# Optimization experiments

Measured on AMD Instinct MI355X. Metric: run time of the kernel, lower is better.

Reference implementation:

```python
import jax, jax.numpy as jnp
import numpy as np
from jax import lax

RATIOS = (0.5, 1.0, 2.0)
SCALES = (8, 16, 32)
BASE = 16
STRIDE = 16
N_PRE = 6000
N_POST = 300      # post-NMS proposals kept
NMS_THRESH = 0.7
MIN_SIZE = 16.0


def _anchor_base():
    x = y = BASE / 2.0
    ab = np.zeros((len(RATIOS) * len(SCALES), 4), np.float32)
    for i, r in enumerate(RATIOS):
        for j, s in enumerate(SCALES):
            h = BASE * s * np.sqrt(r)
            w = BASE * s * np.sqrt(1.0 / r)
            k = i * len(SCALES) + j
            ab[k] = [y - h / 2, x - w / 2, y + h / 2, x + w / 2]
    return ab


def _anchors(h, w):
    ab = _anchor_base()
    sy = np.arange(0, h * STRIDE, STRIDE)
    sx = np.arange(0, w * STRIDE, STRIDE)
    sx, sy = np.meshgrid(sx, sy)
    shift = np.stack((sy.ravel(), sx.ravel(), sy.ravel(), sx.ravel()), axis=1)
    # [K, A, 4] -> [K*A, 4], row-major over (y, x) pixels matching NHWC flatten
    return (ab[None, :, :] + shift[:, None, :]).reshape(-1, 4).astype(np.float32)


def _conv(x, w, b, pad):
    y = lax.conv_general_dilated(x, w, (1, 1), ((pad, pad), (pad, pad)),
                                 dimension_numbers=('NCHW', 'OIHW', 'NCHW'))
    return y + b[None, :, None, None]


def _loc2bbox(anchor, loc):
    h = anchor[:, 2] - anchor[:, 0]
    w = anchor[:, 3] - anchor[:, 1]
    cy = anchor[:, 0] + 0.5 * h
    cx = anchor[:, 1] + 0.5 * w
    dy, dx, dh, dw = loc[:, 0], loc[:, 1], loc[:, 2], loc[:, 3]
    ncy = dy * h + cy
    ncx = dx * w + cx
    nh = jnp.exp(dh) * h
    nw = jnp.exp(dw) * w
    return jnp.stack([ncy - 0.5 * nh, ncx - 0.5 * nw, ncy + 0.5 * nh, ncx + 0.5 * nw], axis=1)


def _iou(b):
    tl = jnp.maximum(b[:, None, :2], b[None, :, :2])
    br = jnp.minimum(b[:, None, 2:], b[None, :, 2:])
    wh = jnp.clip(br - tl, 0.0)
    inter = wh[..., 0] * wh[..., 1]
    area = (b[:, 2] - b[:, 0]) * (b[:, 3] - b[:, 1])
    return inter / (area[:, None] + area[None, :] - inter + 1e-9)


def _nms_keep(iou):
    # greedy NMS over score-sorted boxes: suppress later boxes overlapping kept earlier ones
    n = iou.shape[0]
    idx = jnp.arange(n)
    def step(keep, i):
        sup = (iou[i] > NMS_THRESH) & (idx > i) & keep[i]
        return keep & (~sup), None
    keep, _ = lax.scan(step, jnp.ones((n,), dtype=bool), idx)
    return keep


def _proposal(loc, fg, anchor, img_h, img_w, scale=1.0):
    boxes = _loc2bbox(anchor, loc)
    boxes = jnp.stack([jnp.clip(boxes[:, 0], 0.0, img_h),
                       jnp.clip(boxes[:, 1], 0.0, img_w),
                       jnp.clip(boxes[:, 2], 0.0, img_h),
                       jnp.clip(boxes[:, 3], 0.0, img_w)], axis=1)
    hs = boxes[:, 2] - boxes[:, 0]
    ws = boxes[:, 3] - boxes[:, 1]
    ms = MIN_SIZE * scale
    score = jnp.where((hs >= ms) & (ws >= ms), fg, -jnp.inf)
    top, idx = lax.top_k(score, N_PRE)
    bk = boxes[idx]                                    # [N_PRE, 4]
    keep = _nms_keep(_iou(lax.stop_gradient(bk)))      # selection is non-differentiable
    fs = jnp.where(keep, top, -jnp.inf)
    _, o2 = lax.top_k(fs, N_POST)
    return bk[o2]                                      # [N_POST, 4]


def setup_inputs() -> dict:
    key = jax.random.key(0)
    ks = jax.random.split(key, 4)
    C, H, W = 512, 50, 76
    return {
        "feature": jax.random.normal(ks[0], (1, C, H, W), jnp.float32),
        "conv1_w": jax.random.normal(ks[1], (512, C, 3, 3), jnp.float32) * 0.01,
        "conv1_b": jnp.zeros((512,), jnp.float32),
        "score_w": jax.random.normal(ks[2], (18, 512, 1, 1), jnp.float32) * 0.01,
        "score_b": jnp.zeros((18,), jnp.float32),
        "loc_w": jax.random.normal(ks[3], (36, 512, 1, 1), jnp.float32) * 0.01,
        "loc_b": jnp.zeros((36,), jnp.float32),
        "img_h": 800,
        "img_w": 1216,
    }


def reference(feature, conv1_w, conv1_b, score_w, score_b, loc_w, loc_b, img_h, img_w):
    _, c, h, w = feature.shape
    A = 9
    anchor = jnp.asarray(_anchors(h, w))
    x = jax.nn.relu(_conv(feature, conv1_w, conv1_b, 1))
    locs = _conv(x, loc_w, loc_b, 0)
    rpn_locs = locs.transpose(0, 2, 3, 1).reshape(1, -1, 4)
    sc = _conv(x, score_w, score_b, 0).transpose(0, 2, 3, 1)   # [1, h, w, 2A]
    sm = jax.nn.softmax(sc.reshape(1, h, w, A, 2), axis=-1)
    fg = sm[..., 1].reshape(-1)
    rpn_scores = sc.reshape(1, -1, 2)
    rois = _proposal(rpn_locs[0], fg, anchor, float(img_h), float(img_w), scale=1.0)
    return rpn_locs, rpn_scores, rois, anchor
```

## Files before the change

### kernel.cpp

```cpp
#include <hip/hip_runtime.h>

#define HH 50
#define WW2 76
#define NPIX 3800
#define CIN 512
#define NANCH 34200
#define NPRE 6000
#define NPOST 300
#define WPR 94

typedef unsigned long long u64;
typedef unsigned int u32;

__device__ __forceinline__ int PADL(int i) { return i + (i >> 4); }

template <bool DOW>
__global__ __launch_bounds__(256) void rpn_wtrans(const float* __restrict__ wgt,
                                                  float* __restrict__ wt,
                                                  const float* __restrict__ sw,
                                                  const float* __restrict__ lw,
                                                  float* __restrict__ wt2,
                                                  u32* __restrict__ hist,
                                                  u32* __restrict__ info) {
    __shared__ float tile[32][33];
    const int bx = blockIdx.x;
    const int by = blockIdx.y;
    const int t  = threadIdx.x;
    const int tx = t & 31, ty = t >> 5;
    int gid = (by * 144 + bx) * 256 + t;
    if (gid < 65536) hist[gid] = 0u;
    else if (gid < 65552) info[gid - 65536] = 0u;
    if (gid < 32768) {
        int c = gid >> 6, n = gid & 63;
        float v = 0.f;
        if (n < 18) v = sw[n * 512 + c];
        else if (n < 54) v = lw[(n - 18) * 512 + c];
        wt2[((c >> 2) * 64 + n) * 4 + (c & 3)] = v;
    }
    if (!DOW) return;
#pragma unroll
    for (int r = 0; r < 32; r += 8) {
        int ko = by * 32 + ty + r;
        tile[ty + r][tx] = wgt[(size_t)ko * 4608 + bx * 32 + tx];
    }
    __syncthreads();
#pragma unroll
    for (int r = 0; r < 32; r += 8) {
        int cit = bx * 32 + ty + r;
        wt[(size_t)cit * 512 + by * 32 + tx] = tile[tx][ty + r];
    }
}

template <bool USEWT>
__global__ __launch_bounds__(256, 4) void rpn_conv1(
    const float* __restrict__ feat, const float* __restrict__ wsrc,
    float* __restrict__ Xp, int cin_blk) {
    const int yb = blockIdx.x;
    const int kg = blockIdx.y;
    const int cz = blockIdx.z;
    const int t  = threadIdx.x;
    const int kp = t & 31;
    const int ty = t >> 5;
    const int row  = ty >> 2;
    const int xseg = ty & 3;
    const int x0 = xseg * 20;
    __shared__ float in_l[2816];
    __shared__ float w_l[4608];

    const int y0 = yb * 2 - 1;
    int inSrc[11]; u32 inValid = 0, inPad = 0;
#pragma unroll
    for (int k = 0; k < 11; ++k) {
        int q = t + k * 256;
        int c = q / 336, rem = q - c * 336;
        int r = rem / 84, xx = rem - r * 84;
        int gy = y0 + r, gx = xx - 1;
        bool inb = q < 2688;
        bool ok = inb && ((unsigned)gy < 50u) && ((unsigned)gx < 76u);
        inSrc[k] = c * NPIX + gy * 76 + gx;
        if (ok) inValid |= (1u << k);
        else if (inb) inPad |= (1u << k);
    }
#pragma unroll
    for (int k = 0; k < 11; ++k)
        if ((inPad >> k) & 1) in_l[t + k * 256] = 0.f;

    const float* wb;
    int wOffA = 0;
    int wSrc[18];
    if (USEWT) {
        wb = wsrc + (size_t)(cz * cin_blk) * 9 * 512 + kg * 64;
        wOffA = 8 * t - 7 * (t & 63);
    } else {
        wb = wsrc + (size_t)(kg * 64) * 4608 + (size_t)(cz * cin_blk) * 9;
#pragma unroll
        for (int k = 0; k < 18; ++k) {
            int q = t + k * 256;
            int c = q / 576, r2 = q - c * 576;
            int tap = r2 >> 6, ko = r2 & 63;
            wSrc[k] = ko * 4608 + c * 9 + tap;
        }
    }

    const float* fb = feat + (size_t)(cz * cin_blk) * NPIX;
    float acc0[20], acc1[20];
#pragma unroll
    for (int p = 0; p < 20; ++p) { acc0[p] = 0.f; acc1[p] = 0.f; }

    const int niter = cin_blk >> 3;
#pragma unroll 1
    for (int it = 0; it < niter; ++it) {
        __syncthreads();
#pragma unroll
        for (int k = 0; k < 11; ++k)
            if ((inValid >> k) & 1) in_l[t + k * 256] = fb[inSrc[k]];
        if (USEWT) {
#pragma unroll
            for (int k = 0; k < 18; ++k)
                w_l[t + k * 256] = wb[wOffA + k * 2048];
        } else {
#pragma unroll
            for (int k = 0; k < 18; ++k)
                w_l[t + k * 256] = wb[wSrc[k]];
        }
        __syncthreads();
#pragma unroll 1
        for (int c = 0; c < 8; ++c) {
            const float* ir0 = &in_l[(c * 4 + row) * 84 + x0];
            const float* wl  = &w_l[c * 576 + 2 * kp];
#pragma unroll
            for (int r = 0; r < 3; ++r) {
                const float* ir = ir0 + r * 84;
                float win[22];
#pragma unroll
                for (int w = 0; w < 22; ++w) win[w] = ir[w];
                float w00 = wl[(r * 3 + 0) * 64],     w01 = wl[(r * 3 + 1) * 64],     w02 = wl[(r * 3 + 2) * 64];
                float w10 = wl[(r * 3 + 0) * 64 + 1], w11 = wl[(r * 3 + 1) * 64 + 1], w12 = wl[(r * 3 + 2) * 64 + 1];
#pragma unroll
                for (int p = 0; p < 20; ++p) {
                    acc0[p] = fmaf(w00, win[p],     acc0[p]);
                    acc0[p] = fmaf(w01, win[p + 1], acc0[p]);
                    acc0[p] = fmaf(w02, win[p + 2], acc0[p]);
                    acc1[p] = fmaf(w10, win[p],     acc1[p]);
                    acc1[p] = fmaf(w11, win[p + 1], acc1[p]);
                    acc1[p] = fmaf(w12, win[p + 2], acc1[p]);
                }
            }
        }
        fb += 8 * NPIX;
        wb += USEWT ? 8 * 9 * 512 : 72;
    }

    const int k0 = kg * 64 + 2 * kp;
    const int y = yb * 2 + row;
    float* d0 = Xp + ((size_t)cz * 512 + k0) * NPIX + y * 76 + x0;
#pragma unroll
    for (int p = 0; p < 20; p += 2) {
        if (x0 + p + 1 < 76) {
            *reinterpret_cast<float2*>(d0 + p)        = make_float2(acc0[p], acc0[p + 1]);
            *reinterpret_cast<float2*>(d0 + NPIX + p) = make_float2(acc1[p], acc1[p + 1]);
        }
    }
}

__global__ __launch_bounds__(256) void rpn_combine(
    const float* __restrict__ Xp, const float* __restrict__ bias,
    float* __restrict__ Xt, int nz) {
    const int p0 = blockIdx.x * 256;
    const int c0 = blockIdx.y * 16;
    const int t  = threadIdx.x;
    __shared__ float s[16][257];
    const int p = p0 + t;
#pragma unroll 4
    for (int i = 0; i < 16; ++i) {
        float v = 0.f;
        if (p < NPIX) {
            size_t base = (size_t)(c0 + i) * NPIX + p;
            float a = bias[c0 + i];
            for (int z = 0; z < nz; ++z) a += Xp[(size_t)z * 512 * NPIX + base];
            v = fmaxf(a, 0.f);
        }
        s[i][t] = v;
    }
    __syncthreads();
    const int cs = (t & 3) * 4;
    const int pr = t >> 2;
#pragma unroll
    for (int q = 0; q < 4; ++q) {
        int p2 = p0 + pr + q * 64;
        if (p2 < NPIX) {
            int pi = pr + q * 64;
            float4 v = make_float4(s[cs][pi], s[cs + 1][pi], s[cs + 2][pi], s[cs + 3][pi]);
            *reinterpret_cast<float4*>(&Xt[(size_t)p2 * 512 + c0 + cs]) = v;
        }
    }
}

__global__ __launch_bounds__(64) void rpn_head(
    const float* __restrict__ Xt, const float* __restrict__ wt2,
    const float* __restrict__ sb, const float* __restrict__ lb,
    const int* __restrict__ ihp, const int* __restrict__ iwp,
    float* __restrict__ out, float* __restrict__ boxes,
    u32* __restrict__ keys, u32* __restrict__ hist) {
    const int p0 = blockIdx.x * 8;
    const int t  = threadIdx.x;
    __shared__ __align__(16) float xs[8 * 512];
    __shared__ float ovl[8][64];
    const float4* src = reinterpret_cast<const float4*>(Xt + (size_t)p0 * 512);
    float4* dst = reinterpret_cast<float4*>(xs);
#pragma unroll
    for (int i = 0; i < 16; ++i) dst[t + i * 64] = src[t + i * 64];
    __syncthreads();
    float acc[8];
    {
        float b = (t < 18) ? sb[t] : ((t < 54) ? lb[t - 18] : 0.f);
#pragma unroll
        for (int px = 0; px < 8; ++px) acc[px] = b;
    }
    const float4* wv = reinterpret_cast<const float4*>(wt2) + t;
#pragma unroll 4
    for (int c4 = 0; c4 < 128; ++c4) {
        float4 w = wv[c4 * 64];
#pragma unroll
        for (int px = 0; px < 8; ++px) {
            float4 x = *reinterpret_cast<const float4*>(xs + px * 512 + c4 * 4);
            acc[px] = fmaf(w.x, x.x, acc[px]);
            acc[px] = fmaf(w.y, x.y, acc[px]);
            acc[px] = fmaf(w.z, x.z, acc[px]);
            acc[px] = fmaf(w.w, x.w, acc[px]);
        }
    }
#pragma unroll
    for (int px = 0; px < 8; ++px) ovl[px][t] = acc[px];
    __syncthreads();
    const float ch = (float)(*ihp), cw = (float)(*iwp);
#pragma unroll
    for (int pass = 0; pass < 2; ++pass) {
        int a, px;
        bool act;
        if (pass == 0) { act = (t < 63); px = t / 9; a = t - px * 9; }
        else           { act = (t < 9);  px = 7;     a = t; }
        if (act) {
            const int p = p0 + px;
            const float* ov = ovl[px];
            const float s0 = ov[2 * a], s1 = ov[2 * a + 1];
            const float dy = ov[18 + 4 * a], dx = ov[18 + 4 * a + 1];
            const float dh = ov[18 + 4 * a + 2], dw = ov[18 + 4 * a + 3];
            const int yy = p / WW2, xx = p % WW2;
            const int ai = p * 9 + a;
            *reinterpret_cast<float4*>(out + ai * 4) = make_float4(dy, dx, dh, dw);
            *reinterpret_cast<float2*>(out + 136800 + ai * 2) = make_float2(s0, s1);
            double r  = (a < 3) ? 0.5 : (a < 6) ? 1.0 : 2.0;
            int m3 = a % 3;
            double s2 = (m3 == 0) ? 8.0 : (m3 == 1) ? 16.0 : 32.0;
            double hd = (16.0 * s2) * sqrt(r);
            double wd = (16.0 * s2) * sqrt(1.0 / r);
            float ay1 = (float)(8.0 - hd * 0.5), ax1 = (float)(8.0 - wd * 0.5);
            float ay2 = (float)(8.0 + hd * 0.5), ax2 = (float)(8.0 + wd * 0.5);
            float fy = (float)(yy * 16), fx = (float)(xx * 16);
            float A0 = ay1 + fy, A1 = ax1 + fx, A2 = ay2 + fy, A3 = ax2 + fx;
            *reinterpret_cast<float4*>(out + 206400 + ai * 4) = make_float4(A0, A1, A2, A3);
            float ah = __fsub_rn(A2, A0), aw = __fsub_rn(A3, A1);
            float cy = __fadd_rn(A0, __fmul_rn(0.5f, ah));
            float cx = __fadd_rn(A1, __fmul_rn(0.5f, aw));
            float ncy = __fadd_rn(__fmul_rn(dy, ah), cy);
            float ncx = __fadd_rn(__fmul_rn(dx, aw), cx);
            float nh = __fmul_rn(expf(dh), ah);
            float nw = __fmul_rn(expf(dw), aw);
            float b0 = __fsub_rn(ncy, __fmul_rn(0.5f, nh));
            float b1 = __fsub_rn(ncx, __fmul_rn(0.5f, nw));
            float b2 = __fadd_rn(ncy, __fmul_rn(0.5f, nh));
            float b3 = __fadd_rn(ncx, __fmul_rn(0.5f, nw));
            b0 = fminf(fmaxf(b0, 0.f), ch); b2 = fminf(fmaxf(b2, 0.f), ch);
            b1 = fminf(fmaxf(b1, 0.f), cw); b3 = fminf(fmaxf(b3, 0.f), cw);
            float hs = __fsub_rn(b2, b0), wsz = __fsub_rn(b3, b1);
            float m = fmaxf(s0, s1);
            float e0 = expf(__fsub_rn(s0, m)), e1 = expf(__fsub_rn(s1, m));
            float fg = __fdiv_rn(e1, __fadd_rn(e0, e1));
            float score = (hs >= 16.f && wsz >= 16.f) ? fg : -__builtin_inff();
            *reinterpret_cast<float4*>(boxes + ai * 4) = make_float4(b0, b1, b2, b3);
            u32 kb = __float_as_uint(score);
            kb = (kb & 0x80000000u) ? ~kb : (kb | 0x80000000u);
            keys[ai] = kb;
            atomicAdd(&hist[kb >> 16], 1u);
        }
    }
}

__global__ __launch_bounds__(1024) void rpn_threshsel(const u32* __restrict__ hist,
                                                      u32* __restrict__ info,
                                                      const u32* __restrict__ keys,
                                                      u64* __restrict__ selk) {
    __shared__ u32 tmp[1024];
    __shared__ u32 part[256], h2[256];
    __shared__ int segs;
    __shared__ u32 Tsh;
    const int t = threadIdx.x;
    {
        u32 s = 0;
        const u32* hp = hist + t * 64;
#pragma unroll 8
        for (int b = 0; b < 64; ++b) s += hp[b];
        tmp[t] = s;
    }
    __syncthreads();
    if (t < 256) part[t] = tmp[4 * t] + tmp[4 * t + 1] + tmp[4 * t + 2] + tmp[4 * t + 3];
    __syncthreads();
    for (int off = 1; off < 256; off <<= 1) {
        u32 v = 0, add = 0;
        if (t < 256) { v = part[t]; add = (t + off < 256) ? part[t + off] : 0u; }
        __syncthreads();
        if (t < 256) part[t] = v + add;
        __syncthreads();
    }
    if (t < 256) {
        u32 suf  = part[t];
        u32 sufn = (t < 255) ? part[t + 1] : 0u;
        if (suf >= NPRE && sufn < NPRE) segs = t;
    }
    __syncthreads();
    const int seg = segs;
    const u32 above = (seg < 255) ? part[seg + 1] : 0u;
    if (t < 256) h2[t] = hist[seg * 256 + t];
    __syncthreads();
    for (int off = 1; off < 256; off <<= 1) {
        u32 v = 0, add = 0;
        if (t < 256) { v = h2[t]; add = (t + off < 256) ? h2[t + off] : 0u; }
        __syncthreads();
        if (t < 256) h2[t] = v + add;
        __syncthreads();
    }
    if (t < 256) {
        u32 tot  = above + h2[t];
        u32 totn = above + ((t < 255) ? h2[t + 1] : 0u);
        if (tot >= NPRE && totn < NPRE) Tsh = (u32)(seg * 256 + t);
    }
    __syncthreads();
    const u32 T = Tsh;
    const int lane = t & 63;
    for (int base = 0; base < NANCH; base += 1024) {
        int idx = base + t;
        u32 k = (idx < NANCH) ? keys[idx] : 0u;
        bool sel = (idx < NANCH) && ((k >> 16) >= T);
        u64 ball = __ballot(sel);
        u32 wbase = 0;
        if (lane == 0 && ball) wbase = atomicAdd(&info[2], (u32)__popcll(ball));
        wbase = __shfl(wbase, 0);
        if (sel) {
            u32 pos = wbase + (u32)__popcll(ball & ((1ull << lane) - 1ull));
            if (pos < 8192) selk[pos] = ((u64)k << 32) | (u64)(0xFFFFFFFFu - (u32)idx);
        }
    }
}

__global__ __launch_bounds__(1024) void rpn_sort_local(u64* __restrict__ selk,
                                                       const u32* __restrict__ info) {
    __shared__ u64 s[2176];
    const int t = threadIdx.x;
    const int seg = blockIdx.x;
    const int base = seg * 2048;
    int n = (int)info[2]; if (n > 8192) n = 8192;
    for (int i = t; i < 2048; i += 1024)
        s[PADL(i)] = (base + i < n) ? selk[base + i] : 0ull;
    __syncthreads();
    const bool D = ((seg & 1) == 0);
    for (int k = 2; k <= 2048; k <<= 1) {
        for (int j = k >> 1; j > 0; j >>= 1) {
            int p1 = ((t & ~(j - 1)) << 1) | (t & (j - 1));
            int p2 = p1 | j;
            bool desc = (((p1 & k) == 0) == D);
            u64 A = s[PADL(p1)], B = s[PADL(p2)];
            if (desc ? (A < B) : (A > B)) { s[PADL(p1)] = B; s[PADL(p2)] = A; }
            __syncthreads();
        }
    }
    for (int i = t; i < 2048; i += 1024) selk[base + i] = s[PADL(i)];
}

__global__ __launch_bounds__(1024) void rpn_sort_merge(const u64* __restrict__ selk,
                                                       const float* __restrict__ boxes,
                                                       float* __restrict__ bk) {
    __shared__ u64 s[8192];
    const int t = threadIdx.x;
    for (int i = t; i < 8192; i += 1024) s[i] = selk[i];
    __syncthreads();
    for (int j = 2048; j > 0; j >>= 1) {
#pragma unroll 4
        for (int z = 0; z < 4; ++z) {
            int pi = t + z * 1024;
            int p1 = ((pi & ~(j - 1)) << 1) | (pi & (j - 1));
            int p2 = p1 | j;
            bool desc = ((p1 & 4096) == 0);
            u64 A = s[p1], B = s[p2];
            if (desc ? (A < B) : (A > B)) { s[p1] = B; s[p2] = A; }
        }
        __syncthreads();
    }
    for (int j = 4096; j > 0; j >>= 1) {
#pragma unroll 4
        for (int z = 0; z < 4; ++z) {
            int pi = t + z * 1024;
            int p1 = ((pi & ~(j - 1)) << 1) | (pi & (j - 1));
            int p2 = p1 | j;
            u64 A = s[p1], B = s[p2];
            if (A < B) { s[p1] = B; s[p2] = A; }
        }
        __syncthreads();
    }
    for (int i = t; i < NPRE; i += 1024) {
        u32 oi = 0xFFFFFFFFu - (u32)(s[i] & 0xFFFFFFFFull);
        if (oi >= NANCH) oi = 0;
        reinterpret_cast<float4*>(bk)[i] = reinterpret_cast<const float4*>(boxes)[oi];
    }
}

__global__ __launch_bounds__(64) void rpn_iou(const float* __restrict__ bk,
                                              u64* __restrict__ mask) {
    const int t = threadIdx.x;
    const int bj = blockIdx.x, bi = blockIdx.y;
    const int j0 = bj * 64;
    const int i = bi * 64 + t;
    if (j0 + 63 <= bi * 64) {
        if (i < NPRE) mask[(size_t)i * WPR + bj] = 0ull;
        return;
    }
    __shared__ float4 jb[64];
    jb[t] = (j0 + t < NPRE) ? reinterpret_cast<const float4*>(bk)[j0 + t]
                            : make_float4(0.f, 0.f, 0.f, 0.f);
    __syncthreads();
    if (i >= NPRE) return;
    float4 b = reinterpret_cast<const float4*>(bk)[i];
    float areai = __fmul_rn(__fsub_rn(b.z, b.x), __fsub_rn(b.w, b.y));
    u64 bits = 0ull;
    for (int jj = 0; jj < 64; ++jj) {
        int j = j0 + jj;
        if (j <= i || j >= NPRE) continue;
        float4 c = jb[jj];
        float ty = fmaxf(b.x, c.x), tx = fmaxf(b.y, c.y);
        float by = fminf(b.z, c.z), bx2 = fminf(b.w, c.w);
        float ih = fmaxf(__fsub_rn(by, ty), 0.f);
        float iw = fmaxf(__fsub_rn(bx2, tx), 0.f);
        float inter = __fmul_rn(ih, iw);
        float areaj = __fmul_rn(__fsub_rn(c.z, c.x), __fsub_rn(c.w, c.y));
        float denom = __fadd_rn(__fsub_rn(__fadd_rn(areai, areaj), inter), 1e-9f);
        float iou = __fdiv_rn(inter, denom);
        if (iou > 0.7f) bits |= (1ull << jj);
    }
    mask[(size_t)i * WPR + bj] = bits;
}

__global__ __launch_bounds__(64) void rpn_nms(const u64* __restrict__ mask,
                                              const float* __restrict__ bk,
                                              float* __restrict__ rois) {
    const int lane = threadIdx.x;
    u64 rem0 = 0ull, rem1 = 0ull, curW = 0ull;
    __shared__ unsigned short klist[304];
    int kcnt = 0;
    u64 pm0[16], pm1[16], pmg[16];
#pragma unroll
    for (int u = 0; u < 16; ++u) {
        pm0[u] = mask[(size_t)u * WPR + lane];
        pm1[u] = (lane < 30) ? mask[(size_t)u * WPR + 64 + lane] : 0ull;
        pmg[u] = mask[(size_t)u * WPR + 0];
    }
    bool done = false;
    for (int base = 0; base < NPRE && !done; base += 16) {
        if ((base & 63) == 0) {
            int w = base >> 6;
            curW = (w < 64) ? __shfl(rem0, w) : __shfl(rem1, w - 64);
        }
#pragma unroll
        for (int u = 0; u < 16; ++u) {
            const int i = base + u;
            u64 m0 = pm0[u], m1 = pm1[u], mg = pmg[u];
            const int ni = i + 16;
            pm0[u] = mask[(size_t)ni * WPR + lane];
            pm1[u] = (lane < 30) ? mask[(size_t)ni * WPR + 64 + lane] : 0ull;
            pmg[u] = mask[(size_t)ni * WPR + (ni >> 6)];
            if (((curW >> (i & 63)) & 1ull) == 0ull) {
                rem0 |= m0;
                rem1 |= m1;
                curW |= mg;
                if (lane == 0 && kcnt < 304) klist[kcnt] = (unsigned short)i;
                ++kcnt;
                if (kcnt >= NPOST) { done = true; break; }
            }
        }
    }
    __syncthreads();
    const int nk = kcnt < NPOST ? kcnt : NPOST;
    for (int r = lane; r < nk; r += 64) {
        int bi = klist[r];
        reinterpret_cast<float4*>(rois)[r] = reinterpret_cast<const float4*>(bk)[bi];
    }
    if (kcnt < NPOST) {
        int pos = kcnt;
        for (int i = 0; i < NPRE && pos < NPOST; ++i) {
            int w = i >> 6;
            u64 wv = (w < 64) ? __shfl(rem0, w) : __shfl(rem1, w - 64);
            if ((wv >> (i & 63)) & 1ull) {
                if (lane < 4) rois[pos * 4 + lane] = bk[i * 4 + lane];
                ++pos;
            }
        }
    }
}

extern "C" void kernel_launch(void* const* d_in, const int* in_sizes, int n_in,
                              void* d_out, int out_size, void* d_ws, size_t ws_size,
                              hipStream_t stream) {
    (void)in_sizes; (void)n_in; (void)out_size;
    const float* feat = (const float*)d_in[0];
    const float* w1   = (const float*)d_in[1];
    const float* b1   = (const float*)d_in[2];
    const float* sw   = (const float*)d_in[3];
    const float* sb   = (const float*)d_in[4];
    const float* lw   = (const float*)d_in[5];
    const float* lb   = (const float*)d_in[6];
    const int*   ih   = (const int*)d_in[7];
    const int*   iw   = (const int*)d_in[8];
    float* out = (float*)d_out;

    const size_t WT_B    = 9437184;
    const size_t WT2_B   = 131072;
    const size_t XT_B    = 7782400;
    const size_t REST_B  = WT2_B + 547200 + 136800 + 262144 + 64 + 65536 + 96000 + 4528128;
    const size_t SLICE_B = (size_t)512 * NPIX * 4;
    int nz; bool usewt;
    if      (ws_size >= 8 * SLICE_B + WT_B + XT_B + REST_B) { nz = 8; usewt = true; }
    else if (ws_size >= 4 * SLICE_B + WT_B + XT_B + REST_B) { nz = 4; usewt = true; }
    else if (ws_size >= 2 * SLICE_B + WT_B + XT_B + REST_B) { nz = 2; usewt = true; }
    else                                                    { nz = 2; usewt = false; }

    char* p = (char*)d_ws;
    float* Xp = (float*)p;           p += (size_t)nz * SLICE_B;
    float* wt = nullptr;
    if (usewt) { wt = (float*)p;     p += WT_B; }
    float* Xt     = (float*)p;       p += XT_B;
    float* wt2    = (float*)p;       p += WT2_B;
    float* boxes  = (float*)p;       p += 547200;
    u32*   keys   = (u32*)p;         p += 136800;
    u32*   hist   = (u32*)p;         p += 262144;
    u32*   info   = (u32*)p;         p += 64;
    u64*   selk   = (u64*)p;         p += 65536;
    float* bk     = (float*)p;       p += 96000;
    u64*   mask   = (u64*)p;

    const int cin_blk = 512 / nz;

    if (usewt) {
        rpn_wtrans<true><<<dim3(144, 16), 256, 0, stream>>>(w1, wt, sw, lw, wt2, hist, info);
        rpn_conv1<true><<<dim3(25, 8, nz), 256, 0, stream>>>(feat, wt, Xp, cin_blk);
    } else {
        rpn_wtrans<false><<<dim3(144, 16), 256, 0, stream>>>(w1, nullptr, sw, lw, wt2, hist, info);
        rpn_conv1<false><<<dim3(25, 8, nz), 256, 0, stream>>>(feat, w1, Xp, cin_blk);
    }
    rpn_combine<<<dim3(15, 32), 256, 0, stream>>>(Xp, b1, Xt, nz);
    rpn_head<<<475, 64, 0, stream>>>(Xt, wt2, sb, lb, ih, iw, out, boxes, keys, hist);
    rpn_threshsel<<<1, 1024, 0, stream>>>(hist, info, keys, selk);
    rpn_sort_local<<<4, 1024, 0, stream>>>(selk, info);
    rpn_sort_merge<<<1, 1024, 0, stream>>>(selk, boxes, bk);
    rpn_iou<<<dim3(WPR, WPR), 64, 0, stream>>>(bk, mask);
    rpn_nms<<<1, 64, 0, stream>>>(mask, bk, out + 205200);
}
```

Baseline: 640.0 us.

## Halve conv1 LDS tiles for occupancy and fuse top-k select and sort into one kernel

The conv1 kernel now stages 4 input channels per iteration instead of 8, which halves its shared-memory tiles and raises the launch-bounds occupancy hint from 4 to 8 blocks. The cost is twice as many barrier-separated load phases. Separately, threshold selection, the four-block local bitonic sort and the single-block merge are fused into one kernel. That kernel keeps the selected keys in padded LDS and runs a full 8192-element bitonic sort there, removing two launches and the global round-trip of the selection buffer. The trade-off is that the whole sort now runs on a single workgroup.

```diff
diff --git a/kernel.cpp b/kernel.cpp
--- a/kernel.cpp
+++ b/kernel.cpp
@@ -52,7 +52,7 @@
 }
 
 template <bool USEWT>
-__global__ __launch_bounds__(256, 4) void rpn_conv1(
+__global__ __launch_bounds__(256, 8) void rpn_conv1(
     const float* __restrict__ feat, const float* __restrict__ wsrc,
     float* __restrict__ Xp, int cin_blk) {
     const int yb = blockIdx.x;
@@ -64,37 +64,37 @@
     const int row  = ty >> 2;
     const int xseg = ty & 3;
     const int x0 = xseg * 20;
-    __shared__ float in_l[2816];
-    __shared__ float w_l[4608];
+    __shared__ float in_l[1408];
+    __shared__ float w_l[2304];
 
     const int y0 = yb * 2 - 1;
-    int inSrc[11]; u32 inValid = 0, inPad = 0;
-#pragma unroll
-    for (int k = 0; k < 11; ++k) {
+    int inSrc[6]; u32 inValid = 0, inPad = 0;
+#pragma unroll
+    for (int k = 0; k < 6; ++k) {
         int q = t + k * 256;
         int c = q / 336, rem = q - c * 336;
         int r = rem / 84, xx = rem - r * 84;
         int gy = y0 + r, gx = xx - 1;
-        bool inb = q < 2688;
+        bool inb = q < 1344;
         bool ok = inb && ((unsigned)gy < 50u) && ((unsigned)gx < 76u);
         inSrc[k] = c * NPIX + gy * 76 + gx;
         if (ok) inValid |= (1u << k);
         else if (inb) inPad |= (1u << k);
     }
 #pragma unroll
-    for (int k = 0; k < 11; ++k)
+    for (int k = 0; k < 6; ++k)
         if ((inPad >> k) & 1) in_l[t + k * 256] = 0.f;
 
     const float* wb;
     int wOffA = 0;
-    int wSrc[18];
+    int wSrc[9];
     if (USEWT) {
         wb = wsrc + (size_t)(cz * cin_blk) * 9 * 512 + kg * 64;
         wOffA = 8 * t - 7 * (t & 63);
     } else {
         wb = wsrc + (size_t)(kg * 64) * 4608 + (size_t)(cz * cin_blk) * 9;
 #pragma unroll
-        for (int k = 0; k < 18; ++k) {
+        for (int k = 0; k < 9; ++k) {
             int q = t + k * 256;
             int c = q / 576, r2 = q - c * 576;
             int tap = r2 >> 6, ko = r2 & 63;
@@ -107,25 +107,25 @@
 #pragma unroll
     for (int p = 0; p < 20; ++p) { acc0[p] = 0.f; acc1[p] = 0.f; }
 
-    const int niter = cin_blk >> 3;
+    const int niter = cin_blk >> 2;
 #pragma unroll 1
     for (int it = 0; it < niter; ++it) {
         __syncthreads();
 #pragma unroll
-        for (int k = 0; k < 11; ++k)
+        for (int k = 0; k < 6; ++k)
             if ((inValid >> k) & 1) in_l[t + k * 256] = fb[inSrc[k]];
         if (USEWT) {
 #pragma unroll
-            for (int k = 0; k < 18; ++k)
+            for (int k = 0; k < 9; ++k)
                 w_l[t + k * 256] = wb[wOffA + k * 2048];
         } else {
 #pragma unroll
-            for (int k = 0; k < 18; ++k)
+            for (int k = 0; k < 9; ++k)
                 w_l[t + k * 256] = wb[wSrc[k]];
         }
         __syncthreads();
 #pragma unroll 1
-        for (int c = 0; c < 8; ++c) {
+        for (int c = 0; c < 4; ++c) {
             const float* ir0 = &in_l[(c * 4 + row) * 84 + x0];
             const float* wl  = &w_l[c * 576 + 2 * kp];
 #pragma unroll
@@ -147,8 +147,8 @@
                 }
             }
         }
-        fb += 8 * NPIX;
-        wb += USEWT ? 8 * 9 * 512 : 72;
+        fb += 4 * NPIX;
+        wb += USEWT ? 4 * 9 * 512 : 36;
     }
 
     const int k0 = kg * 64 + 2 * kp;
@@ -287,24 +287,29 @@
     }
 }
 
-__global__ __launch_bounds__(1024) void rpn_threshsel(const u32* __restrict__ hist,
-                                                      u32* __restrict__ info,
-                                                      const u32* __restrict__ keys,
-                                                      u64* __restrict__ selk) {
-    __shared__ u32 tmp[1024];
+__global__ __launch_bounds__(1024) void rpn_topk(const u32* __restrict__ hist,
+                                                 const u32* __restrict__ keys,
+                                                 const float* __restrict__ boxes,
+                                                 float* __restrict__ bk) {
+    __shared__ u64 s[8704];
     __shared__ u32 part[256], h2[256];
     __shared__ int segs;
-    __shared__ u32 Tsh;
+    __shared__ u32 Tsh, cnt;
     const int t = threadIdx.x;
+    if (t == 0) cnt = 0u;
+    u32* tmp = (u32*)s;
     {
-        u32 s = 0;
+        u32 sum = 0;
         const u32* hp = hist + t * 64;
 #pragma unroll 8
-        for (int b = 0; b < 64; ++b) s += hp[b];
-        tmp[t] = s;
-    }
-    __syncthreads();
-    if (t < 256) part[t] = tmp[4 * t] + tmp[4 * t + 1] + tmp[4 * t + 2] + tmp[4 * t + 3];
+        for (int b = 0; b < 64; ++b) sum += hp[b];
+        tmp[t] = sum;
+    }
+    __syncthreads();
+    u32 p4 = 0;
+    if (t < 256) p4 = tmp[4 * t] + tmp[4 * t + 1] + tmp[4 * t + 2] + tmp[4 * t + 3];
+    __syncthreads();
+    if (t < 256) part[t] = p4;
     __syncthreads();
     for (int off = 1; off < 256; off <<= 1) {
         u32 v = 0, add = 0;
@@ -344,71 +349,36 @@
         bool sel = (idx < NANCH) && ((k >> 16) >= T);
         u64 ball = __ballot(sel);
         u32 wbase = 0;
-        if (lane == 0 && ball) wbase = atomicAdd(&info[2], (u32)__popcll(ball));
+        if (lane == 0 && ball) wbase = atomicAdd(&cnt, (u32)__popcll(ball));
         wbase = __shfl(wbase, 0);
         if (sel) {
             u32 pos = wbase + (u32)__popcll(ball & ((1ull << lane) - 1ull));
-            if (pos < 8192) selk[pos] = ((u64)k << 32) | (u64)(0xFFFFFFFFu - (u32)idx);
-        }
-    }
-}
-
-__global__ __launch_bounds__(1024) void rpn_sort_local(u64* __restrict__ selk,
-                                                       const u32* __restrict__ info) {
-    __shared__ u64 s[2176];
-    const int t = threadIdx.x;
-    const int seg = blockIdx.x;
-    const int base = seg * 2048;
-    int n = (int)info[2]; if (n > 8192) n = 8192;
-    for (int i = t; i < 2048; i += 1024)
-        s[PADL(i)] = (base + i < n) ? selk[base + i] : 0ull;
-    __syncthreads();
-    const bool D = ((seg & 1) == 0);
-    for (int k = 2; k <= 2048; k <<= 1) {
+            if (pos < 8192) s[PADL((int)pos)] = ((u64)k << 32) | (u64)(0xFFFFFFFFu - (u32)idx);
+        }
+    }
+    __syncthreads();
+    {
+        int n = (int)cnt; if (n > 8192) n = 8192;
+        for (int i = t; i < 8192; i += 1024)
+            if (i >= n) s[PADL(i)] = 0ull;
+    }
+    __syncthreads();
+    for (int k = 2; k <= 8192; k <<= 1) {
         for (int j = k >> 1; j > 0; j >>= 1) {
-            int p1 = ((t & ~(j - 1)) << 1) | (t & (j - 1));
-            int p2 = p1 | j;
-            bool desc = (((p1 & k) == 0) == D);
-            u64 A = s[PADL(p1)], B = s[PADL(p2)];
-            if (desc ? (A < B) : (A > B)) { s[PADL(p1)] = B; s[PADL(p2)] = A; }
+#pragma unroll 4
+            for (int z = 0; z < 4; ++z) {
+                int pi = t + z * 1024;
+                int p1 = ((pi & ~(j - 1)) << 1) | (pi & (j - 1));
+                int p2 = p1 | j;
+                bool desc = ((p1 & k) == 0);
+                u64 A = s[PADL(p1)], B = s[PADL(p2)];
+                if (desc ? (A < B) : (A > B)) { s[PADL(p1)] = B; s[PADL(p2)] = A; }
+            }
             __syncthreads();
         }
     }
-    for (int i = t; i < 2048; i += 1024) selk[base + i] = s[PADL(i)];
-}
-
-__global__ __launch_bounds__(1024) void rpn_sort_merge(const u64* __restrict__ selk,
-                                                       const float* __restrict__ boxes,
-                                                       float* __restrict__ bk) {
-    __shared__ u64 s[8192];
-    const int t = threadIdx.x;
-    for (int i = t; i < 8192; i += 1024) s[i] = selk[i];
-    __syncthreads();
-    for (int j = 2048; j > 0; j >>= 1) {
-#pragma unroll 4
-        for (int z = 0; z < 4; ++z) {
-            int pi = t + z * 1024;
-            int p1 = ((pi & ~(j - 1)) << 1) | (pi & (j - 1));
-            int p2 = p1 | j;
-            bool desc = ((p1 & 4096) == 0);
-            u64 A = s[p1], B = s[p2];
-            if (desc ? (A < B) : (A > B)) { s[p1] = B; s[p2] = A; }
-        }
-        __syncthreads();
-    }
-    for (int j = 4096; j > 0; j >>= 1) {
-#pragma unroll 4
-        for (int z = 0; z < 4; ++z) {
-            int pi = t + z * 1024;
-            int p1 = ((pi & ~(j - 1)) << 1) | (pi & (j - 1));
-            int p2 = p1 | j;
-            u64 A = s[p1], B = s[p2];
-            if (A < B) { s[p1] = B; s[p2] = A; }
-        }
-        __syncthreads();
-    }
     for (int i = t; i < NPRE; i += 1024) {
-        u32 oi = 0xFFFFFFFFu - (u32)(s[i] & 0xFFFFFFFFull);
+        u32 oi = 0xFFFFFFFFu - (u32)(s[PADL(i)] & 0xFFFFFFFFull);
         if (oi >= NANCH) oi = 0;
         reinterpret_cast<float4*>(bk)[i] = reinterpret_cast<const float4*>(boxes)[oi];
     }
@@ -524,7 +494,7 @@
     const size_t WT_B    = 9437184;
     const size_t WT2_B   = 131072;
     const size_t XT_B    = 7782400;
-    const size_t REST_B  = WT2_B + 547200 + 136800 + 262144 + 64 + 65536 + 96000 + 4528128;
+    const size_t REST_B  = WT2_B + 547200 + 136800 + 262144 + 64 + 96000 + 4528128;
     const size_t SLICE_B = (size_t)512 * NPIX * 4;
     int nz; bool usewt;
     if      (ws_size >= 8 * SLICE_B + WT_B + XT_B + REST_B) { nz = 8; usewt = true; }
@@ -542,7 +512,6 @@
     u32*   keys   = (u32*)p;         p += 136800;
     u32*   hist   = (u32*)p;         p += 262144;
     u32*   info   = (u32*)p;         p += 64;
-    u64*   selk   = (u64*)p;         p += 65536;
     float* bk     = (float*)p;       p += 96000;
     u64*   mask   = (u64*)p;
 
@@ -557,9 +526,7 @@
     }
     rpn_combine<<<dim3(15, 32), 256, 0, stream>>>(Xp, b1, Xt, nz);
     rpn_head<<<475, 64, 0, stream>>>(Xt, wt2, sb, lb, ih, iw, out, boxes, keys, hist);
-    rpn_threshsel<<<1, 1024, 0, stream>>>(hist, info, keys, selk);
-    rpn_sort_local<<<4, 1024, 0, stream>>>(selk, info);
-    rpn_sort_merge<<<1, 1024, 0, stream>>>(selk, boxes, bk);
+    rpn_topk<<<1, 1024, 0, stream>>>(hist, keys, boxes, bk);
     rpn_iou<<<dim3(WPR, WPR), 64, 0, stream>>>(bk, mask);
     rpn_nms<<<1, 64, 0, stream>>>(mask, bk, out + 205200);
 }
```

Measured after the change: 1.929 ms. 201% more time.
